# Kernel optimization log

Measured on AMD Instinct MI355X. Metric: run time of the kernel, lower is better.

Reference implementation:

```python
import jax, jax.numpy as jnp
import numpy as np

D_MODEL = 1024
NUM_HEADS = 16
D_K = D_MODEL // NUM_HEADS
SCALE = 1.0 / np.sqrt(D_K).astype(np.float32)
NEG_INF = -1.0e9


def setup_inputs() -> dict:
    key = jax.random.key(0)
    ks = jax.random.split(key, 9)
    B, S = 4, 2048
    query = jax.random.normal(ks[0], (B, S, D_MODEL), dtype=jnp.float32)
    key_t = jax.random.normal(ks[1], (B, S, D_MODEL), dtype=jnp.float32)
    value = jax.random.normal(ks[2], (B, S, D_MODEL), dtype=jnp.float32)
    mask = jax.random.randint(ks[3], (B, S), 0, 2, dtype=jnp.int32)
    init = 1.0 / np.sqrt(D_MODEL).astype(np.float32)
    W_q = jax.random.uniform(ks[4], (D_MODEL, D_MODEL), jnp.float32, -init, init)
    W_k = jax.random.uniform(ks[5], (D_MODEL, D_MODEL), jnp.float32, -init, init)
    W_v = jax.random.uniform(ks[6], (D_MODEL, D_MODEL), jnp.float32, -init, init)
    W_o = jax.random.uniform(ks[7], (D_MODEL, D_MODEL), jnp.float32, -init, init)
    b_o = jax.random.uniform(ks[8], (D_MODEL,), jnp.float32, -init, init)
    return {"query": query, "key": key_t, "value": value, "mask": mask,
            "W_q": W_q, "W_k": W_k, "W_v": W_v, "W_o": W_o, "b_o": b_o}


def reference(query, key, value, mask, W_q, W_k, W_v, W_o, b_o):
    B, S, _ = query.shape
    # projections -> [B, H, S, d_k]  (torch Linear: x @ W.T)
    def split_heads(x, W):
        y = jnp.einsum('bsd,ed->bse', x, W)
        return y.reshape(B, S, NUM_HEADS, D_K).transpose(0, 2, 1, 3)
    Q = split_heads(query, W_q)
    K = split_heads(key, W_k)
    V = split_heads(value, W_v)
    # scores [B, H, S, S]
    scores = jnp.einsum('bhqd,bhkd->bhqk', Q, K) * SCALE
    key_mask = (mask[:, None, None, :] != 0)  # [B,1,1,S] over key axis
    scores = jnp.where(key_mask, scores, NEG_INF)
    probs = jax.nn.softmax(scores, axis=-1)
    # dropout is identity (p=0 / eval mode)
    context = jnp.einsum('bhqk,bhkd->bhqd', probs, V)
    context = context.transpose(0, 2, 1, 3).reshape(B, S, D_MODEL)
    output = jnp.einsum('bsd,ed->bse', context, W_o) + b_o
    return output, probs.mean(axis=1)
```

## Files before the change

### kernel.cpp

```cpp
#include <hip/hip_runtime.h>

typedef unsigned short u16t;
typedef __bf16 bf16x8 __attribute__((ext_vector_type(8)));
typedef float f32x4 __attribute__((ext_vector_type(4)));

#define NB 4
#define NS 2048
#define ND 1024
#define NH 16
#define NDK 64
#define NEGINF -1.0e9f
#define SCALE2 0.18033688011112042f

#define LAB 40

__device__ __forceinline__ float fexp2(float x) { return __builtin_amdgcn_exp2f(x); }

__device__ __forceinline__ u16t f2bf(float f) {
  return __builtin_bit_cast(u16t, (__bf16)f);
}

#define ROR16(x, n) __builtin_bit_cast(float, __builtin_amdgcn_update_dpp(     \
    __builtin_bit_cast(int, (x)), __builtin_bit_cast(int, (x)),                \
    0x120 + (n), 0xF, 0xF, false))

__device__ __forceinline__ int swz(int row, int col) {
  return row * 64 + (col ^ ((row & 7) << 3));
}

template<typename TA> struct Stg;
template<> struct Stg<float> {
  f32x4 lo, hi;
  __device__ __forceinline__ void ld(const float* p) {
    lo = *(const f32x4*)p; hi = *(const f32x4*)(p + 4);
  }
  __device__ __forceinline__ bf16x8 get() const {
    bf16x8 r;
    r[0] = (__bf16)lo[0]; r[1] = (__bf16)lo[1]; r[2] = (__bf16)lo[2]; r[3] = (__bf16)lo[3];
    r[4] = (__bf16)hi[0]; r[5] = (__bf16)hi[1]; r[6] = (__bf16)hi[2]; r[7] = (__bf16)hi[3];
    return r;
  }
};
template<> struct Stg<u16t> {
  bf16x8 v;
  __device__ __forceinline__ void ld(const u16t* p) { v = *(const bf16x8*)p; }
  __device__ __forceinline__ bf16x8 get() const { return v; }
};

template<typename TA, int MODE>
__global__ __launch_bounds__(256, 2)
void gemm_nt(const TA* __restrict__ A, const float* __restrict__ Bm,
             void* __restrict__ Cv, const float* __restrict__ bias)
{
  const int K = 1024;
  __shared__ __attribute__((aligned(16))) u16t At[128 * LAB];
  __shared__ __attribute__((aligned(16))) u16t Bt[128 * LAB];

  const int tid  = threadIdx.x;
  const int w    = tid >> 6;
  const int lane = tid & 63;
  const int quad = lane >> 4;
  const int l16  = lane & 15;
  const int wm   = w >> 1, wn = w & 1;
  const int m0   = blockIdx.x * 128;
  const int n0   = blockIdx.y * 128;

  const f32x4 fz = {0.f, 0.f, 0.f, 0.f};
  f32x4 acc[4][4];
#pragma unroll
  for (int i = 0; i < 4; i++)
#pragma unroll
    for (int j = 0; j < 4; j++) acc[i][j] = fz;

  const int r0 = tid >> 2, cg = (tid & 3) * 8;
  const int r1 = r0 + 64;

  Stg<TA> sa0, sa1; Stg<float> sb0, sb1;
  sa0.ld(A  + (long)(m0 + r0) * K + cg);
  sa1.ld(A  + (long)(m0 + r1) * K + cg);
  sb0.ld(Bm + (long)(n0 + r0) * K + cg);
  sb1.ld(Bm + (long)(n0 + r1) * K + cg);

  for (int k0 = 0; k0 < K; k0 += 32) {
    __syncthreads();
    *(bf16x8*)&At[r0 * LAB + cg] = sa0.get();
    *(bf16x8*)&At[r1 * LAB + cg] = sa1.get();
    *(bf16x8*)&Bt[r0 * LAB + cg] = sb0.get();
    *(bf16x8*)&Bt[r1 * LAB + cg] = sb1.get();
    __syncthreads();
    if (k0 + 32 < K) {
      sa0.ld(A  + (long)(m0 + r0) * K + k0 + 32 + cg);
      sa1.ld(A  + (long)(m0 + r1) * K + k0 + 32 + cg);
      sb0.ld(Bm + (long)(n0 + r0) * K + k0 + 32 + cg);
      sb1.ld(Bm + (long)(n0 + r1) * K + k0 + 32 + cg);
    }

    bf16x8 af[4], bfv[4];
#pragma unroll
    for (int i = 0; i < 4; i++)
      af[i] = *(const bf16x8*)&At[(wm * 64 + i * 16 + l16) * LAB + quad * 8];
#pragma unroll
    for (int j = 0; j < 4; j++)
      bfv[j] = *(const bf16x8*)&Bt[(wn * 64 + j * 16 + l16) * LAB + quad * 8];
#pragma unroll
    for (int i = 0; i < 4; i++)
#pragma unroll
      for (int j = 0; j < 4; j++)
        acc[i][j] = __builtin_amdgcn_mfma_f32_16x16x32_bf16(af[i], bfv[j], acc[i][j], 0, 0, 0);
  }

#pragma unroll
  for (int i = 0; i < 4; i++) {
    const int rbase = m0 + wm * 64 + i * 16 + quad * 4;
#pragma unroll
    for (int j = 0; j < 4; j++) {
      const int col = n0 + wn * 64 + j * 16 + l16;
      float bv = 0.f;
      if (MODE == 0) bv = bias[col];
#pragma unroll
      for (int r = 0; r < 4; r++) {
        const int row = rbase + r;
        float v = acc[i][j][r];
        if (MODE == 0) {
          ((float*)Cv)[(long)row * ND + col] = v + bv;
        } else if (MODE == 1) {
          int b = row >> 11, s = row & 2047, h = col >> 6, d = col & 63;
          ((u16t*)Cv)[(((long)(b * NH + h)) * NS + s) * NDK + d] = f2bf(v);
        } else {
          int b = row >> 11, s = row & 2047, h = col >> 6, d = col & 63;
          ((u16t*)Cv)[(((long)(b * NH + h)) * NDK + d) * NS + s] = f2bf(v);
        }
      }
    }
  }
}

__global__ __launch_bounds__(512, 4)
void flash_ctx(const u16t* __restrict__ Qw, const u16t* __restrict__ Kw,
               const u16t* __restrict__ VTw, const int* __restrict__ mask,
               u16t* __restrict__ ctx, float* __restrict__ mo, float* __restrict__ lo)
{
  __shared__ __attribute__((aligned(16))) u16t Kt[64 * 64];
  __shared__ __attribute__((aligned(16))) u16t Vt[64 * 64];
  __shared__ __attribute__((aligned(16))) u16t Pt[8 * 16 * 64];
  __shared__ float biasl[NS];

  const int tid  = threadIdx.x;
  const int w    = tid >> 6;
  const int lane = tid & 63;
  const int quad = lane >> 4;
  const int l16  = lane & 15;
  const int bh   = blockIdx.y;
  const int b    = bh >> 4;
  const int h    = bh & 15;
  const int qw   = blockIdx.x * 128 + w * 16;
  const int pbase = w * 1024;

  for (int i = tid; i < NS; i += 512)
    biasl[i] = mask[b * NS + i] ? 0.f : NEGINF;

  bf16x8 qf[2];
#pragma unroll
  for (int kk = 0; kk < 2; kk++)
    qf[kk] = *(const bf16x8*)(Qw + ((long)bh * NS + qw + l16) * NDK + kk * 32 + quad * 8);

  const f32x4 fz = {0.f, 0.f, 0.f, 0.f};
  const f32x4 fm = {NEGINF, NEGINF, NEGINF, NEGINF};
  f32x4 cacc[4];
#pragma unroll
  for (int d = 0; d < 4; d++) cacc[d] = fz;
  f32x4 mrun = fm;
  f32x4 lrun = fz;

  const int kr0 = tid >> 3, kc0 = (tid & 7) * 8;
  const long kbase = (long)bh * NS;
  const long vbase = (long)bh * NDK;

  bf16x8 kv = *(const bf16x8*)(Kw  + (kbase + kr0) * NDK + kc0);
  bf16x8 vv = *(const bf16x8*)(VTw + (vbase + kr0) * NS + kc0);

  for (int kb = 0; kb < NS; kb += 64) {
    __syncthreads();
    *(bf16x8*)&Kt[swz(kr0, kc0)] = kv;
    *(bf16x8*)&Vt[swz(kr0, kc0)] = vv;
    __syncthreads();
    if (kb + 64 < NS) {
      kv = *(const bf16x8*)(Kw  + (kbase + kb + 64 + kr0) * NDK + kc0);
      vv = *(const bf16x8*)(VTw + (vbase + kr0) * NS + kb + 64 + kc0);
    }

    f32x4 s[4];
#pragma unroll
    for (int c = 0; c < 4; c++) {
      f32x4 a = fz;
#pragma unroll
      for (int kk = 0; kk < 2; kk++) {
        bf16x8 kf = *(const bf16x8*)&Kt[swz(c * 16 + l16, kk * 32 + quad * 8)];
        a = __builtin_amdgcn_mfma_f32_16x16x32_bf16(qf[kk], kf, a, 0, 0, 0);
      }
      s[c] = a;
    }

#pragma unroll
    for (int c = 0; c < 4; c++) {
      const float bias_c = biasl[kb + c * 16 + l16];
#pragma unroll
      for (int r = 0; r < 4; r++)
        s[c][r] = s[c][r] * SCALE2 + bias_c;
    }

    f32x4 mx = s[0];
#pragma unroll
    for (int c = 1; c < 4; c++)
#pragma unroll
      for (int r = 0; r < 4; r++) mx[r] = fmaxf(mx[r], s[c][r]);
#pragma unroll
    for (int r = 0; r < 4; r++) {
      float x = mx[r];
      x = fmaxf(x, ROR16(x, 1));
      x = fmaxf(x, ROR16(x, 2));
      x = fmaxf(x, ROR16(x, 4));
      x = fmaxf(x, ROR16(x, 8));
      mx[r] = x;
    }

    f32x4 alpha;
#pragma unroll
    for (int r = 0; r < 4; r++) {
      float mnew = fmaxf(mrun[r], mx[r]);
      alpha[r] = fexp2(mrun[r] - mnew);
      mrun[r] = mnew;
    }
#pragma unroll
    for (int c = 0; c < 4; c++)
#pragma unroll
      for (int r = 0; r < 4; r++) s[c][r] = fexp2(s[c][r] - mrun[r]);

    f32x4 sm = fz;
#pragma unroll
    for (int c = 0; c < 4; c++)
#pragma unroll
      for (int r = 0; r < 4; r++) sm[r] += s[c][r];
#pragma unroll
    for (int r = 0; r < 4; r++) {
      float x = sm[r];
      x += ROR16(x, 1);
      x += ROR16(x, 2);
      x += ROR16(x, 4);
      x += ROR16(x, 8);
      sm[r] = x;
    }
#pragma unroll
    for (int r = 0; r < 4; r++) lrun[r] = lrun[r] * alpha[r] + sm[r];
#pragma unroll
    for (int d = 0; d < 4; d++)
#pragma unroll
      for (int r = 0; r < 4; r++) cacc[d][r] *= alpha[r];

#pragma unroll
    for (int c = 0; c < 4; c++)
#pragma unroll
      for (int r = 0; r < 4; r++)
        Pt[pbase + swz(quad * 4 + r, c * 16 + l16)] = f2bf(s[c][r]);

#pragma unroll
    for (int d = 0; d < 4; d++)
#pragma unroll
      for (int kk = 0; kk < 2; kk++) {
        bf16x8 pf = *(const bf16x8*)&Pt[pbase + swz(l16, kk * 32 + quad * 8)];
        bf16x8 vf = *(const bf16x8*)&Vt[swz(d * 16 + l16, kk * 32 + quad * 8)];
        cacc[d] = __builtin_amdgcn_mfma_f32_16x16x32_bf16(pf, vf, cacc[d], 0, 0, 0);
      }
  }

  {
    f32x4 rinv;
#pragma unroll
    for (int r = 0; r < 4; r++) rinv[r] = 1.f / lrun[r];
#pragma unroll
    for (int d = 0; d < 4; d++)
#pragma unroll
      for (int r = 0; r < 4; r++) {
        int qg = qw + quad * 4 + r;
        int e  = h * NDK + d * 16 + l16;
        ctx[((long)(b * NS + qg)) * ND + e] = f2bf(cacc[d][r] * rinv[r]);
      }
    if (l16 == 0) {
#pragma unroll
      for (int r = 0; r < 4; r++) {
        int qg = qw + quad * 4 + r;
        mo[(long)bh * NS + qg] = mrun[r];
        lo[(long)bh * NS + qg] = lrun[r];
      }
    }
  }
}

__global__ __launch_bounds__(256, 3)
void probs_mean(const u16t* __restrict__ Qw, const u16t* __restrict__ Kw,
                const int* __restrict__ mask, const float* __restrict__ mo,
                const float* __restrict__ lo, float* __restrict__ outp)
{
  __shared__ __attribute__((aligned(16))) u16t Qt[128 * 64];
  __shared__ __attribute__((aligned(16))) u16t Kt2[128 * 64];
  __shared__ float ml[NH * 128];
  __shared__ float li[NH * 128];
  __shared__ float biasl[128];

  const int tid  = threadIdx.x;
  const int w    = tid >> 6;
  const int lane = tid & 63;
  const int quad = lane >> 4;
  const int l16  = lane & 15;
  const int wm   = w >> 1, wn = w & 1;
  const int b  = blockIdx.z;
  const int q0 = blockIdx.y * 128;
  const int k0 = blockIdx.x * 128;

  for (int i = tid; i < NH * 128; i += 256) {
    int hh = i >> 7, r = i & 127;
    ml[i] = mo[((long)(b * NH + hh)) * NS + q0 + r];
    li[i] = 1.f / lo[((long)(b * NH + hh)) * NS + q0 + r];
  }
  for (int i = tid; i < 128; i += 256)
    biasl[i] = mask[b * NS + k0 + i] ? 0.f : NEGINF;

  const f32x4 fz = {0.f, 0.f, 0.f, 0.f};
  f32x4 acc[4][4];
#pragma unroll
  for (int i = 0; i < 4; i++)
#pragma unroll
    for (int j = 0; j < 4; j++) acc[i][j] = fz;

  bf16x8 qv[4], kv[4];
#pragma unroll
  for (int rr = 0; rr < 4; rr++) {
    int idx = rr * 256 + tid;
    int row = idx >> 3, off = (idx & 7) * 8;
    qv[rr] = *(const bf16x8*)(Qw + ((long)(b * NH) * NS + q0 + row) * NDK + off);
    kv[rr] = *(const bf16x8*)(Kw + ((long)(b * NH) * NS + k0 + row) * NDK + off);
  }

  for (int hh = 0; hh < NH; hh++) {
    __syncthreads();
#pragma unroll
    for (int rr = 0; rr < 4; rr++) {
      int idx = rr * 256 + tid;
      int row = idx >> 3, off = (idx & 7) * 8;
      *(bf16x8*)&Qt[swz(row, off)]  = qv[rr];
      *(bf16x8*)&Kt2[swz(row, off)] = kv[rr];
    }
    __syncthreads();
    if (hh + 1 < NH) {
#pragma unroll
      for (int rr = 0; rr < 4; rr++) {
        int idx = rr * 256 + tid;
        int row = idx >> 3, off = (idx & 7) * 8;
        qv[rr] = *(const bf16x8*)(Qw + ((long)(b * NH + hh + 1) * NS + q0 + row) * NDK + off);
        kv[rr] = *(const bf16x8*)(Kw + ((long)(b * NH + hh + 1) * NS + k0 + row) * NDK + off);
      }
    }

    bf16x8 af[4][2], bfv[4][2];
#pragma unroll
    for (int i = 0; i < 4; i++)
#pragma unroll
      for (int kk = 0; kk < 2; kk++) {
        af[i][kk]  = *(const bf16x8*)&Qt[swz(wm * 64 + i * 16 + l16, kk * 32 + quad * 8)];
        bfv[i][kk] = *(const bf16x8*)&Kt2[swz(wn * 64 + i * 16 + l16, kk * 32 + quad * 8)];
      }
#pragma unroll
    for (int i = 0; i < 4; i++)
#pragma unroll
      for (int j = 0; j < 4; j++) {
        f32x4 s = fz;
#pragma unroll
        for (int kk = 0; kk < 2; kk++)
          s = __builtin_amdgcn_mfma_f32_16x16x32_bf16(af[i][kk], bfv[j][kk], s, 0, 0, 0);
        const float bias_c = biasl[wn * 64 + j * 16 + l16];
#pragma unroll
        for (int r = 0; r < 4; r++) {
          int rowb = wm * 64 + i * 16 + quad * 4 + r;
          float p = fexp2(s[r] * SCALE2 + bias_c - ml[hh * 128 + rowb]) * li[hh * 128 + rowb];
          acc[i][j][r] += p;
        }
      }
  }

#pragma unroll
  for (int i = 0; i < 4; i++)
#pragma unroll
    for (int j = 0; j < 4; j++)
#pragma unroll
      for (int r = 0; r < 4; r++) {
        int row = q0 + wm * 64 + i * 16 + quad * 4 + r;
        int col = k0 + wn * 64 + j * 16 + l16;
        outp[((long)(b * NS + row)) * NS + col] = acc[i][j][r] * (1.f / 16.f);
      }
}

extern "C" void kernel_launch(void* const* d_in, const int* in_sizes, int n_in,
                              void* d_out, int out_size, void* d_ws, size_t ws_size,
                              hipStream_t stream)
{
  (void)in_sizes; (void)n_in; (void)out_size; (void)ws_size;
  const float* query = (const float*)d_in[0];
  const float* keyt  = (const float*)d_in[1];
  const float* value = (const float*)d_in[2];
  const int*   mask  = (const int*)d_in[3];
  const float* Wq = (const float*)d_in[4];
  const float* Wk = (const float*)d_in[5];
  const float* Wv = (const float*)d_in[6];
  const float* Wo = (const float*)d_in[7];
  const float* bo = (const float*)d_in[8];

  float* out  = (float*)d_out;
  float* outp = out + (long)NB * NS * ND;

  u16t* q_ws  = (u16t*)d_ws;
  u16t* k_ws  = q_ws + (long)NB * NH * NS * NDK;
  u16t* vt_ws = k_ws + (long)NB * NH * NS * NDK;
  float* m_ws = (float*)(vt_ws + (long)NB * NH * NS * NDK);
  float* l_ws = m_ws + (long)NB * NH * NS;
  u16t* ctx_ws = (u16t*)outp;

  dim3 blk(256);
  gemm_nt<float, 1><<<dim3(64, 8), blk, 0, stream>>>(query, Wq, q_ws, nullptr);
  gemm_nt<float, 1><<<dim3(64, 8), blk, 0, stream>>>(keyt,  Wk, k_ws, nullptr);
  gemm_nt<float, 2><<<dim3(64, 8), blk, 0, stream>>>(value, Wv, vt_ws, nullptr);
  flash_ctx<<<dim3(NS / 128, NB * NH), dim3(512), 0, stream>>>(q_ws, k_ws, vt_ws, mask,
                                                               ctx_ws, m_ws, l_ws);
  gemm_nt<u16t, 0><<<dim3(64, 8), blk, 0, stream>>>(ctx_ws, Wo, out, bo);
  probs_mean<<<dim3(NS / 128, NS / 128, NB), blk, 0, stream>>>(q_ws, k_ws, mask,
                                                               m_ws, l_ws, outp);
}
```

Baseline: 518.3 us.

## Process 128-key blocks per iteration in flash attention kernel

The key/value tile per loop iteration in the flash-attention kernel doubles from 64 to 128 keys. Each thread now loads two 8-element chunks of K and of V^T, V gets a wider swizzled LDS layout, and P@V runs in two halves that reuse the per-wave P buffer. The aim is to halve the number of __syncthreads barriers and online-softmax rescale steps per key, and to give more MFMA work per iteration. In exchange, K/V shared memory doubles, which can cut how many blocks fit on a CU, and the larger score array raises register pressure.

Result: slower. 533.5 us (+2.9%).

```diff
diff --git a/kernel.cpp b/kernel.cpp
--- a/kernel.cpp
+++ b/kernel.cpp
@@ -26,6 +26,9 @@
 
 __device__ __forceinline__ int swz(int row, int col) {
   return row * 64 + (col ^ ((row & 7) << 3));
+}
+__device__ __forceinline__ int swzV(int row, int col) {
+  return row * 128 + (col ^ ((row & 7) << 3));
 }
 
 template<typename TA> struct Stg;
@@ -140,8 +143,8 @@
                const u16t* __restrict__ VTw, const int* __restrict__ mask,
                u16t* __restrict__ ctx, float* __restrict__ mo, float* __restrict__ lo)
 {
-  __shared__ __attribute__((aligned(16))) u16t Kt[64 * 64];
-  __shared__ __attribute__((aligned(16))) u16t Vt[64 * 64];
+  __shared__ __attribute__((aligned(16))) u16t Kt[128 * 64];
+  __shared__ __attribute__((aligned(16))) u16t Vt[64 * 128];
   __shared__ __attribute__((aligned(16))) u16t Pt[8 * 16 * 64];
   __shared__ float biasl[NS];
 
@@ -172,26 +175,33 @@
   f32x4 mrun = fm;
   f32x4 lrun = fz;
 
-  const int kr0 = tid >> 3, kc0 = (tid & 7) * 8;
+  const int kr = tid >> 2, kc = (tid & 3) * 16;
+  const int vr = tid >> 3, vc = (tid & 7) * 16;
   const long kbase = (long)bh * NS;
   const long vbase = (long)bh * NDK;
 
-  bf16x8 kv = *(const bf16x8*)(Kw  + (kbase + kr0) * NDK + kc0);
-  bf16x8 vv = *(const bf16x8*)(VTw + (vbase + kr0) * NS + kc0);
-
-  for (int kb = 0; kb < NS; kb += 64) {
-    __syncthreads();
-    *(bf16x8*)&Kt[swz(kr0, kc0)] = kv;
-    *(bf16x8*)&Vt[swz(kr0, kc0)] = vv;
-    __syncthreads();
-    if (kb + 64 < NS) {
-      kv = *(const bf16x8*)(Kw  + (kbase + kb + 64 + kr0) * NDK + kc0);
-      vv = *(const bf16x8*)(VTw + (vbase + kr0) * NS + kb + 64 + kc0);
-    }
-
-    f32x4 s[4];
-#pragma unroll
-    for (int c = 0; c < 4; c++) {
+  bf16x8 kva = *(const bf16x8*)(Kw  + (kbase + kr) * NDK + kc);
+  bf16x8 kvb = *(const bf16x8*)(Kw  + (kbase + kr) * NDK + kc + 8);
+  bf16x8 vva = *(const bf16x8*)(VTw + (vbase + vr) * NS + vc);
+  bf16x8 vvb = *(const bf16x8*)(VTw + (vbase + vr) * NS + vc + 8);
+
+  for (int kb = 0; kb < NS; kb += 128) {
+    __syncthreads();
+    *(bf16x8*)&Kt[swz(kr, kc)]      = kva;
+    *(bf16x8*)&Kt[swz(kr, kc + 8)]  = kvb;
+    *(bf16x8*)&Vt[swzV(vr, vc)]     = vva;
+    *(bf16x8*)&Vt[swzV(vr, vc + 8)] = vvb;
+    __syncthreads();
+    if (kb + 128 < NS) {
+      kva = *(const bf16x8*)(Kw  + (kbase + kb + 128 + kr) * NDK + kc);
+      kvb = *(const bf16x8*)(Kw  + (kbase + kb + 128 + kr) * NDK + kc + 8);
+      vva = *(const bf16x8*)(VTw + (vbase + vr) * NS + kb + 128 + vc);
+      vvb = *(const bf16x8*)(VTw + (vbase + vr) * NS + kb + 128 + vc + 8);
+    }
+
+    f32x4 s[8];
+#pragma unroll
+    for (int c = 0; c < 8; c++) {
       f32x4 a = fz;
 #pragma unroll
       for (int kk = 0; kk < 2; kk++) {
@@ -202,7 +212,7 @@
     }
 
 #pragma unroll
-    for (int c = 0; c < 4; c++) {
+    for (int c = 0; c < 8; c++) {
       const float bias_c = biasl[kb + c * 16 + l16];
 #pragma unroll
       for (int r = 0; r < 4; r++)
@@ -211,7 +221,7 @@
 
     f32x4 mx = s[0];
 #pragma unroll
-    for (int c = 1; c < 4; c++)
+    for (int c = 1; c < 8; c++)
 #pragma unroll
       for (int r = 0; r < 4; r++) mx[r] = fmaxf(mx[r], s[c][r]);
 #pragma unroll
@@ -232,13 +242,13 @@
       mrun[r] = mnew;
     }
 #pragma unroll
-    for (int c = 0; c < 4; c++)
+    for (int c = 0; c < 8; c++)
 #pragma unroll
       for (int r = 0; r < 4; r++) s[c][r] = fexp2(s[c][r] - mrun[r]);
 
     f32x4 sm = fz;
 #pragma unroll
-    for (int c = 0; c < 4; c++)
+    for (int c = 0; c < 8; c++)
 #pragma unroll
       for (int r = 0; r < 4; r++) sm[r] += s[c][r];
 #pragma unroll
@@ -258,19 +268,25 @@
       for (int r = 0; r < 4; r++) cacc[d][r] *= alpha[r];
 
 #pragma unroll
-    for (int c = 0; c < 4; c++)
-#pragma unroll
-      for (int r = 0; r < 4; r++)
-        Pt[pbase + swz(quad * 4 + r, c * 16 + l16)] = f2bf(s[c][r]);
-
-#pragma unroll
-    for (int d = 0; d < 4; d++)
-#pragma unroll
-      for (int kk = 0; kk < 2; kk++) {
-        bf16x8 pf = *(const bf16x8*)&Pt[pbase + swz(l16, kk * 32 + quad * 8)];
-        bf16x8 vf = *(const bf16x8*)&Vt[swz(d * 16 + l16, kk * 32 + quad * 8)];
-        cacc[d] = __builtin_amdgcn_mfma_f32_16x16x32_bf16(pf, vf, cacc[d], 0, 0, 0);
-      }
+    for (int hk = 0; hk < 2; hk++) {
+#pragma unroll
+      for (int c2 = 0; c2 < 4; c2++)
+#pragma unroll
+        for (int r = 0; r < 4; r++)
+          Pt[pbase + swz(quad * 4 + r, c2 * 16 + l16)] = f2bf(s[hk * 4 + c2][r]);
+
+      bf16x8 pf[2];
+#pragma unroll
+      for (int kk = 0; kk < 2; kk++)
+        pf[kk] = *(const bf16x8*)&Pt[pbase + swz(l16, kk * 32 + quad * 8)];
+#pragma unroll
+      for (int d = 0; d < 4; d++)
+#pragma unroll
+        for (int kk = 0; kk < 2; kk++) {
+          bf16x8 vf = *(const bf16x8*)&Vt[swzV(d * 16 + l16, hk * 64 + kk * 32 + quad * 8)];
+          cacc[d] = __builtin_amdgcn_mfma_f32_16x16x32_bf16(pf[kk], vf, cacc[d], 0, 0, 0);
+        }
+    }
   }
 
   {
```
